# Performance work log

Measured on AMD Instinct MI355X. Metric: run time of the kernel, lower is better.

## Reference

```python
import jax, jax.numpy as jnp
import numpy as np

B, T, H, E = 256, 256, 512, 96  # batch, enc seq len, hidden/enc dim, charset size


def setup_inputs() -> dict:
    key = jax.random.key(0)
    ks = jax.random.split(key, 9)
    s = 0.05  # param scale
    return {
        "prev_h": jax.random.normal(ks[0], (B, H), jnp.float32),
        "prev_c": jax.random.normal(ks[1], (B, H), jnp.float32),
        "batch_H": jax.random.normal(ks[2], (B, T, H), jnp.float32),
        "char_onehots": jax.nn.one_hot(jax.random.randint(ks[3], (B,), 0, E), E, dtype=jnp.float32),
        "W_i2h": jax.random.normal(ks[4], (H, H), jnp.float32) * s,
        "W_h2h": jax.random.normal(ks[5], (H, H), jnp.float32) * s,
        "b_h2h": jnp.zeros((H,), jnp.float32),
        "w_score": jax.random.normal(ks[6], (H, 1), jnp.float32) * s,
        "W_lstm": jax.random.normal(ks[7], (H + E, 4 * H), jnp.float32) * s,
        "U_lstm": jax.random.normal(ks[8], (H, 4 * H), jnp.float32) * s,
        "b_lstm": jnp.zeros((4 * H,), jnp.float32),
    }


def reference(prev_h, prev_c, batch_H, char_onehots,
              W_i2h, W_h2h, b_h2h, w_score, W_lstm, U_lstm, b_lstm):
    # Additive (Bahdanau) attention
    proj = jnp.einsum('btd,dh->bth', batch_H, W_i2h)          # [B,T,H]
    hp = prev_h @ W_h2h + b_h2h                               # [B,H]
    e = jnp.tanh(proj + hp[:, None, :]) @ w_score             # [B,T,1]
    alpha = jax.nn.softmax(e, axis=1)                         # [B,T,1]
    context = jnp.einsum('bt,btd->bd', alpha[..., 0], batch_H)  # [B,D]
    x = jnp.concatenate([context, char_onehots], axis=1)      # [B,D+E]
    # Keras LSTMCell: gate order i, f, c(g), o
    z = x @ W_lstm + prev_h @ U_lstm + b_lstm                 # [B,4H]
    i, f, g, o = jnp.split(z, 4, axis=1)
    c_new = jax.nn.sigmoid(f) * prev_c + jax.nn.sigmoid(i) * jnp.tanh(g)
    h_new = jax.nn.sigmoid(o) * jnp.tanh(c_new)
    return h_new, c_new, alpha
```

## Files before the change

kernel.cpp:

```cpp
#include <hip/hip_runtime.h>
#include <hip/hip_bf16.h>
#include <math.h>

#define Bq 256
#define Tq 256
#define Hq 512
#define Eq 96

typedef __attribute__((ext_vector_type(8))) short short8;
typedef __attribute__((ext_vector_type(4))) float f32x4;

static __device__ __forceinline__ unsigned short f2bf(float f) {
  union { float f; unsigned u; } v; v.f = f;
  unsigned r = v.u + 0x7FFF + ((v.u >> 16) & 1);
  return (unsigned short)(r >> 16);
}

static __device__ __forceinline__ ushort4 pack4(float4 v) {
  ushort4 p;
  p.x = f2bf(v.x); p.y = f2bf(v.y); p.z = f2bf(v.z); p.w = f2bf(v.w);
  return p;
}

static __device__ __forceinline__ short8 pack8(float4 a, float4 b) {
  union { short8 s; ushort4 u[2]; } r;
  r.u[0] = pack4(a); r.u[1] = pack4(b);
  return r.s;
}

static __device__ __forceinline__ float sat_tanh(float x) {
  float ax = fminf(fabsf(x), 15.0f);
  float e = __builtin_exp2f(ax * 2.885390082f);
  float t = 1.0f - 2.0f / (e + 1.0f);
  return copysignf(t, x);
}

static __device__ __forceinline__ float sat_sig(float x) {
  float cx = fmaxf(fminf(x, 30.0f), -30.0f);
  return 1.0f / (1.0f + __builtin_exp2f(-cx * 1.442695041f));
}

__global__ __launch_bounds__(256) void convW_k(const float* __restrict__ W,
                                               unsigned short* __restrict__ Wt) {
  __shared__ float tile[32][33];
  int bx = blockIdx.x & 15, by = blockIdx.x >> 4;
  int tx = threadIdx.x & 31, ty = threadIdx.x >> 5;
  #pragma unroll
  for (int i = 0; i < 32; i += 8)
    tile[ty + i][tx] = W[(size_t)(by * 32 + ty + i) * Hq + bx * 32 + tx];
  __syncthreads();
  #pragma unroll
  for (int i = 0; i < 32; i += 8)
    Wt[(size_t)(bx * 32 + ty + i) * Hq + by * 32 + tx] = f2bf(tile[tx][ty + i]);
}

__global__ __launch_bounds__(256) void hsplit_k(const float* __restrict__ ph,
                                                const float* __restrict__ Whh,
                                                float* __restrict__ hp) {
  __shared__ __align__(16) float xs[8][128];
  const int ks = blockIdx.x & 3;
  const int nc = (blockIdx.x >> 2) & 3;
  const int bg = blockIdx.x >> 4;
  const int tid = threadIdx.x;
  const int row0 = bg * 8;
  const int d0 = ks * 128;
  for (int i = tid; i < 8 * 32; i += 256) {
    int r = i >> 5, dd = (i & 31) * 4;
    *(float4*)&xs[r][dd] = *(const float4*)&ph[(size_t)(row0 + r) * Hq + d0 + dd];
  }
  __syncthreads();
  const int rt = tid >> 6;
  const int ct = tid & 63;
  const int n = nc * 128 + ct * 2;
  float a00 = 0, a01 = 0, a10 = 0, a11 = 0;
  for (int dd = 0; dd < 128; dd += 4) {
    float4 x0 = *(const float4*)&xs[rt * 2][dd];
    float4 x1 = *(const float4*)&xs[rt * 2 + 1][dd];
    #pragma unroll
    for (int j = 0; j < 4; j++) {
      float2 w = *(const float2*)&Whh[(size_t)(d0 + dd + j) * Hq + n];
      float xj0 = ((const float*)&x0)[j];
      float xj1 = ((const float*)&x1)[j];
      a00 += xj0 * w.x; a01 += xj0 * w.y;
      a10 += xj1 * w.x; a11 += xj1 * w.y;
    }
  }
  int row = row0 + rt * 2;
  atomicAdd(&hp[(size_t)row * Hq + n], a00);
  atomicAdd(&hp[(size_t)row * Hq + n + 1], a01);
  atomicAdd(&hp[(size_t)(row + 1) * Hq + n], a10);
  atomicAdd(&hp[(size_t)(row + 1) * Hq + n + 1], a11);
}

#define LDKA 72

__global__ __launch_bounds__(512) void fused_score5_k(
    const float* __restrict__ A,
    const unsigned short* __restrict__ Wt,
    const float* __restrict__ hp,
    const float* __restrict__ bh,
    const float* __restrict__ wsc,
    float* __restrict__ e) {
  __shared__ unsigned short As[2][128 * LDKA];
  __shared__ unsigned short Bs[2][128 * LDKA];
  __shared__ float red[8][64];

  const int tid = threadIdx.x;
  const int n0 = blockIdx.x * 128;
  const int m0 = blockIdx.y * 128;
  const int b = m0 >> 8;
  const int wave = tid >> 6;
  const int lane = tid & 63;
  const int quad = lane >> 4;
  const int l16 = lane & 15;
  const int wm = wave >> 2;
  const int wn4 = wave & 3;

  const int arow = tid >> 2, aq = tid & 3;
  const float* Agp = A + (size_t)(m0 + arow) * Hq + aq * 16;
  const unsigned short* Bgp = Wt + (size_t)(n0 + arow) * Hq + aq * 16;

  f32x4 acc[4][2] = {};

  {
    float4 a0[4]; uint4 b0[2];
    #pragma unroll
    for (int q = 0; q < 4; q++) a0[q] = *(const float4*)(Agp + q * 4);
    b0[0] = *(const uint4*)(Bgp);
    b0[1] = *(const uint4*)(Bgp + 8);
    *(short8*)&As[0][arow * LDKA + aq * 16] = pack8(a0[0], a0[1]);
    *(short8*)&As[0][arow * LDKA + aq * 16 + 8] = pack8(a0[2], a0[3]);
    *(uint4*)&Bs[0][arow * LDKA + aq * 16] = b0[0];
    *(uint4*)&Bs[0][arow * LDKA + aq * 16 + 8] = b0[1];
  }
  __syncthreads();

  int cur = 0;
  for (int ks = 0; ks < 8; ks++) {
    float4 aN[4]; uint4 bN[2];
    if (ks < 7) {
      const int k1 = (ks + 1) * 64;
      #pragma unroll
      for (int q = 0; q < 4; q++) aN[q] = *(const float4*)(Agp + k1 + q * 4);
      bN[0] = *(const uint4*)(Bgp + k1);
      bN[1] = *(const uint4*)(Bgp + k1 + 8);
    }

    short8 af[4][2], bf[2][2];
    #pragma unroll
    for (int mi = 0; mi < 4; mi++)
      #pragma unroll
      for (int k2 = 0; k2 < 2; k2++)
        af[mi][k2] = *(const short8*)&As[cur][(wm * 64 + mi * 16 + l16) * LDKA + k2 * 32 + quad * 8];
    #pragma unroll
    for (int ni = 0; ni < 2; ni++)
      #pragma unroll
      for (int k2 = 0; k2 < 2; k2++)
        bf[ni][k2] = *(const short8*)&Bs[cur][(wn4 * 32 + ni * 16 + l16) * LDKA + k2 * 32 + quad * 8];

    #pragma unroll
    for (int k2 = 0; k2 < 2; k2++)
      #pragma unroll
      for (int mi = 0; mi < 4; mi++)
        #pragma unroll
        for (int ni = 0; ni < 2; ni++)
          acc[mi][ni] = __builtin_amdgcn_mfma_f32_16x16x32_bf16(
              af[mi][k2], bf[ni][k2], acc[mi][ni], 0, 0, 0);

    if (ks < 7) {
      *(short8*)&As[cur ^ 1][arow * LDKA + aq * 16] = pack8(aN[0], aN[1]);
      *(short8*)&As[cur ^ 1][arow * LDKA + aq * 16 + 8] = pack8(aN[2], aN[3]);
      *(uint4*)&Bs[cur ^ 1][arow * LDKA + aq * 16] = bN[0];
      *(uint4*)&Bs[cur ^ 1][arow * LDKA + aq * 16 + 8] = bN[1];
    }
    __syncthreads();
    cur ^= 1;
  }

  float hv[2], wv[2];
  #pragma unroll
  for (int ni = 0; ni < 2; ni++) {
    int c = n0 + wn4 * 32 + ni * 16 + l16;
    hv[ni] = hp[(size_t)b * Hq + c] + bh[c];
    wv[ni] = wsc[c];
  }
  #pragma unroll
  for (int mi = 0; mi < 4; mi++) {
    float s[4] = {0, 0, 0, 0};
    #pragma unroll
    for (int ni = 0; ni < 2; ni++)
      #pragma unroll
      for (int r = 0; r < 4; r++)
        s[r] += sat_tanh(acc[mi][ni][r] + hv[ni]) * wv[ni];
    #pragma unroll
    for (int r = 0; r < 4; r++) {
      s[r] += __shfl_xor(s[r], 8, 64);
      s[r] += __shfl_xor(s[r], 4, 64);
      s[r] += __shfl_xor(s[r], 2, 64);
      s[r] += __shfl_xor(s[r], 1, 64);
    }
    if (l16 == 0) {
      #pragma unroll
      for (int r = 0; r < 4; r++) red[wave][mi * 16 + quad * 4 + r] = s[r];
    }
  }
  __syncthreads();
  if (tid < 128) {
    const int half = tid >> 6, ri = tid & 63;
    float t = red[half * 4 + 0][ri] + red[half * 4 + 1][ri] +
              red[half * 4 + 2][ri] + red[half * 4 + 3][ri];
    atomicAdd(&e[m0 + tid], t);
  }
}

__global__ __launch_bounds__(256) void softmax_k(float* __restrict__ ea) {
  __shared__ float red[8];
  int b = blockIdx.x, t = threadIdx.x;
  int wave = t >> 6, lane = t & 63;
  float x = ea[b * Tq + t];
  float m = x;
  #pragma unroll
  for (int off = 32; off >= 1; off >>= 1) m = fmaxf(m, __shfl_xor(m, off, 64));
  if (lane == 0) red[wave] = m;
  __syncthreads();
  m = fmaxf(fmaxf(red[0], red[1]), fmaxf(red[2], red[3]));
  float ex = __builtin_exp2f((x - m) * 1.442695041f);
  float s = ex;
  #pragma unroll
  for (int off = 32; off >= 1; off >>= 1) s += __shfl_xor(s, off, 64);
  if (lane == 0) red[4 + wave] = s;
  __syncthreads();
  s = red[4] + red[5] + red[6] + red[7];
  ea[b * Tq + t] = ex / s;
}

__global__ __launch_bounds__(256) void ctxsplit_k(const float* __restrict__ alpha,
                                                  const float* __restrict__ bH,
                                                  float* __restrict__ ctx) {
  __shared__ float al[64];
  const int b = blockIdx.x >> 2;
  const int tc = blockIdx.x & 3;
  const int tid = threadIdx.x;
  if (tid < 64) al[tid] = alpha[b * Tq + tc * 64 + tid];
  __syncthreads();
  const float2* Hp = (const float2*)(bH + (size_t)b * Tq * Hq + (size_t)tc * 64 * Hq);
  float ax = 0.f, ay = 0.f;
  #pragma unroll 8
  for (int t = 0; t < 64; t++) {
    float a = al[t];
    float2 v = Hp[t * (Hq / 2) + tid];
    ax += a * v.x;
    ay += a * v.y;
  }
  atomicAdd(&ctx[(size_t)b * Hq + 2 * tid], ax);
  atomicAdd(&ctx[(size_t)b * Hq + 2 * tid + 1], ay);
}

__global__ __launch_bounds__(256) void zsplit_k(
    const float* __restrict__ ctx, const float* __restrict__ oneh,
    const float* __restrict__ ph, const float* __restrict__ Wl,
    const float* __restrict__ Ul, float* __restrict__ z) {
  __shared__ __align__(16) float xs[32 * 280];
  const int ks = blockIdx.x & 3;
  const int hc = (blockIdx.x >> 2) & 7;
  const int bg = blockIdx.x >> 5;
  const int tid = threadIdx.x;
  const int row0 = bg * 32;
  const int dbase = ks * 280;

  for (int i = tid; i < 32 * 280; i += 256) {
    int r = i / 280, dd = i % 280;
    int g = dbase + dd;
    float v;
    if (g < 512) v = ctx[(size_t)(row0 + r) * Hq + g];
    else if (g < 608) v = oneh[(row0 + r) * Eq + (g - 512)];
    else v = ph[(size_t)(row0 + r) * Hq + (g - 608)];
    xs[r * 280 + dd] = v;
  }
  __syncthreads();

  const int rt = tid >> 6;
  const int ct = tid & 63;
  const int c0 = ct * 4;
  const int gate = c0 >> 6;
  const int ho = c0 & 63;
  const int n = gate * 512 + hc * 64 + ho;

  float acc[8][4] = {};
  for (int dd = 0; dd < 280; dd += 4) {
    float4 xr[8];
    #pragma unroll
    for (int r = 0; r < 8; r++)
      xr[r] = *(const float4*)&xs[(rt * 8 + r) * 280 + dd];
    #pragma unroll
    for (int j = 0; j < 4; j++) {
      int g = dbase + dd + j;
      const float* wp = (g < 608) ? &Wl[(size_t)g * 2048 + n]
                                  : &Ul[(size_t)(g - 608) * 2048 + n];
      float4 w = *(const float4*)wp;
      #pragma unroll
      for (int r = 0; r < 8; r++) {
        float x = ((const float*)&xr[r])[j];
        acc[r][0] += x * w.x; acc[r][1] += x * w.y;
        acc[r][2] += x * w.z; acc[r][3] += x * w.w;
      }
    }
  }
  #pragma unroll
  for (int r = 0; r < 8; r++) {
    float* zp = &z[(size_t)(row0 + rt * 8 + r) * 2048 + n];
    #pragma unroll
    for (int j = 0; j < 4; j++) atomicAdd(zp + j, acc[r][j]);
  }
}

__global__ __launch_bounds__(256) void gatesz_k(const float* __restrict__ z,
                                                const float* __restrict__ bl,
                                                const float* __restrict__ pc,
                                                float* __restrict__ outh,
                                                float* __restrict__ outc) {
  int p = blockIdx.x * 256 + threadIdx.x;
  #pragma unroll
  for (int q = 0; q < 2; q++, p += 65536) {
    int r = p >> 9, h = p & 511;
    const float* zb = z + (size_t)r * 2048;
    float gi = zb[h] + bl[h];
    float gf = zb[512 + h] + bl[512 + h];
    float gg = zb[1024 + h] + bl[1024 + h];
    float go = zb[1536 + h] + bl[1536 + h];
    float cn = sat_sig(gf) * pc[p] + sat_sig(gi) * sat_tanh(gg);
    float hn = sat_sig(go) * sat_tanh(cn);
    outh[p] = hn;
    outc[p] = cn;
  }
}

#define KXc 1120
__global__ __launch_bounds__(256) void zgates2_k(
    const float* __restrict__ ctx, const float* __restrict__ oneh,
    const float* __restrict__ ph, const float* __restrict__ pc,
    const float* __restrict__ Wl, const float* __restrict__ Ul,
    const float* __restrict__ bl,
    float* __restrict__ outh, float* __restrict__ outc) {
  __shared__ __align__(16) float xs[8 * KXc];
  const int bg = blockIdx.x >> 3;
  const int hc = blockIdx.x & 7;
  const int tid = threadIdx.x;
  const int row0 = bg * 8;

  for (int i = tid; i < 8 * 128; i += 256) {
    int r = i >> 7, dd = (i & 127) * 4;
    *(float4*)&xs[r * KXc + dd] = *(const float4*)&ctx[(size_t)(row0 + r) * Hq + dd];
  }
  for (int i = tid; i < 8 * 128; i += 256) {
    int r = i >> 7, dd = (i & 127) * 4;
    *(float4*)&xs[r * KXc + 608 + dd] = *(const float4*)&ph[(size_t)(row0 + r) * Hq + dd];
  }
  if (tid < 8 * 24) {
    int r = tid / 24, dd = (tid % 24) * 4;
    *(float4*)&xs[r * KXc + 512 + dd] = *(const float4*)&oneh[(row0 + r) * Eq + dd];
  }
  __syncthreads();

  const int rt = tid >> 6;
  const int ct = tid & 63;
  const int c0 = ct * 4;
  const int gate = c0 >> 6;
  const int ho = c0 & 63;
  const int n = gate * 512 + hc * 64 + ho;

  float acc0[4] = {0, 0, 0, 0};
  float acc1[4] = {0, 0, 0, 0};
  const float* xr0 = &xs[(rt * 2) * KXc];
  const float* xr1 = &xs[(rt * 2 + 1) * KXc];

  for (int d = 0; d < 608; d += 4) {
    float4 x0 = *(const float4*)&xr0[d];
    float4 x1 = *(const float4*)&xr1[d];
    #pragma unroll
    for (int j = 0; j < 4; j++) {
      float4 w = *(const float4*)&Wl[(size_t)(d + j) * 2048 + n];
      float a = ((const float*)&x0)[j], b = ((const float*)&x1)[j];
      acc0[0] += a * w.x; acc0[1] += a * w.y; acc0[2] += a * w.z; acc0[3] += a * w.w;
      acc1[0] += b * w.x; acc1[1] += b * w.y; acc1[2] += b * w.z; acc1[3] += b * w.w;
    }
  }
  for (int d = 0; d < 512; d += 4) {
    float4 x0 = *(const float4*)&xr0[608 + d];
    float4 x1 = *(const float4*)&xr1[608 + d];
    #pragma unroll
    for (int j = 0; j < 4; j++) {
      float4 w = *(const float4*)&Ul[(size_t)(d + j) * 2048 + n];
      float a = ((const float*)&x0)[j], b = ((const float*)&x1)[j];
      acc0[0] += a * w.x; acc0[1] += a * w.y; acc0[2] += a * w.z; acc0[3] += a * w.w;
      acc1[0] += b * w.x; acc1[1] += b * w.y; acc1[2] += b * w.z; acc1[3] += b * w.w;
    }
  }

  __syncthreads();
  float* zs = xs;
  #pragma unroll
  for (int j = 0; j < 4; j++) {
    zs[(rt * 2) * 256 + c0 + j] = acc0[j];
    zs[(rt * 2 + 1) * 256 + c0 + j] = acc1[j];
  }
  __syncthreads();

  #pragma unroll
  for (int p = tid; p < 512; p += 256) {
    int r = p >> 6, o = p & 63;
    int h = hc * 64 + o;
    int grow = row0 + r;
    float gi = zs[r * 256 + o]       + bl[h];
    float gf = zs[r * 256 + 64 + o]  + bl[512 + h];
    float gg = zs[r * 256 + 128 + o] + bl[1024 + h];
    float go = zs[r * 256 + 192 + o] + bl[1536 + h];
    float cn = sat_sig(gf) * pc[(size_t)grow * Hq + h] + sat_sig(gi) * sat_tanh(gg);
    float hn = sat_sig(go) * sat_tanh(cn);
    outh[(size_t)grow * Hq + h] = hn;
    outc[(size_t)grow * Hq + h] = cn;
  }
}

extern "C" void kernel_launch(void* const* d_in, const int* in_sizes, int n_in,
                              void* d_out, int out_size, void* d_ws, size_t ws_size,
                              hipStream_t stream) {
  const float* prev_h = (const float*)d_in[0];
  const float* prev_c = (const float*)d_in[1];
  const float* batch_H = (const float*)d_in[2];
  const float* oneh = (const float*)d_in[3];
  const float* W_i2h = (const float*)d_in[4];
  const float* W_h2h = (const float*)d_in[5];
  const float* b_h2h = (const float*)d_in[6];
  const float* w_score = (const float*)d_in[7];
  const float* W_lstm = (const float*)d_in[8];
  const float* U_lstm = (const float*)d_in[9];
  const float* b_lstm = (const float*)d_in[10];

  float* out = (float*)d_out;
  float* outh = out;
  float* outc = out + Bq * Hq;
  float* alpha = out + 2 * Bq * Hq;

  float* ws = (float*)d_ws;
  float* hp = ws;
  float* ctx = ws;
  unsigned short* Wt = (unsigned short*)(ws + 131072);
  float* z = ws + 131072;

  const bool bigws = ws_size >= 2621440;

  hipMemsetAsync(alpha, 0, Bq * Tq * sizeof(float), stream);
  hipMemsetAsync(hp, 0, Bq * Hq * sizeof(float), stream);
  convW_k<<<256, 256, 0, stream>>>(W_i2h, Wt);
  hsplit_k<<<512, 256, 0, stream>>>(prev_h, W_h2h, hp);
  dim3 g5(4, 512);
  fused_score5_k<<<g5, 512, 0, stream>>>(batch_H, Wt, hp, b_h2h, w_score, alpha);
  softmax_k<<<256, 256, 0, stream>>>(alpha);
  if (bigws) {
    hipMemsetAsync(ws, 0, 2621440, stream);
    ctxsplit_k<<<1024, 256, 0, stream>>>(alpha, batch_H, ctx);
    zsplit_k<<<256, 256, 0, stream>>>(ctx, oneh, prev_h, W_lstm, U_lstm, z);
    gatesz_k<<<256, 256, 0, stream>>>(z, b_lstm, prev_c, outh, outc);
  } else {
    hipMemsetAsync(ctx, 0, Bq * Hq * sizeof(float), stream);
    ctxsplit_k<<<1024, 256, 0, stream>>>(alpha, batch_H, ctx);
    zgates2_k<<<256, 256, 0, stream>>>(ctx, oneh, prev_h, prev_c,
                                       W_lstm, U_lstm, b_lstm, outh, outc);
  }
}
```

Measured before the change: 407.4 us.

## Drop atomics in hp GEMM and score partials; remap blocks per XCD

The hidden projection kernel now covers the full K range in each block and writes its results directly, so the memset and float atomics are gone. With a large workspace, the score kernel writes per-N-chunk partial scores to a 4x buffer that a new softmax kernel sums, removing the alpha memset and the atomics there too. Score blocks are remapped on a 1D grid so that consecutive M-tiles, and the four N-chunks sharing each A tile, land on the same XCD for L2 reuse. The trade-offs are fewer, longer hp blocks (128 blocks covering full K) and extra workspace traffic for the partial scores.

```diff
diff --git a/kernel.cpp b/kernel.cpp
--- a/kernel.cpp
+++ b/kernel.cpp
@@ -54,31 +54,29 @@
     Wt[(size_t)(bx * 32 + ty + i) * Hq + by * 32 + tx] = f2bf(tile[tx][ty + i]);
 }
 
-__global__ __launch_bounds__(256) void hsplit_k(const float* __restrict__ ph,
-                                                const float* __restrict__ Whh,
-                                                float* __restrict__ hp) {
-  __shared__ __align__(16) float xs[8][128];
-  const int ks = blockIdx.x & 3;
-  const int nc = (blockIdx.x >> 2) & 3;
-  const int bg = blockIdx.x >> 4;
+__global__ __launch_bounds__(256) void hsplitF_k(const float* __restrict__ ph,
+                                                 const float* __restrict__ Whh,
+                                                 float* __restrict__ hp) {
+  __shared__ __align__(16) float xs[8][512];
+  const int nc = blockIdx.x & 3;
+  const int bg = blockIdx.x >> 2;
   const int tid = threadIdx.x;
   const int row0 = bg * 8;
-  const int d0 = ks * 128;
-  for (int i = tid; i < 8 * 32; i += 256) {
-    int r = i >> 5, dd = (i & 31) * 4;
-    *(float4*)&xs[r][dd] = *(const float4*)&ph[(size_t)(row0 + r) * Hq + d0 + dd];
+  for (int i = tid; i < 8 * 128; i += 256) {
+    int r = i >> 7, dd = (i & 127) * 4;
+    *(float4*)&xs[r][dd] = *(const float4*)&ph[(size_t)(row0 + r) * Hq + dd];
   }
   __syncthreads();
   const int rt = tid >> 6;
   const int ct = tid & 63;
   const int n = nc * 128 + ct * 2;
   float a00 = 0, a01 = 0, a10 = 0, a11 = 0;
-  for (int dd = 0; dd < 128; dd += 4) {
+  for (int dd = 0; dd < 512; dd += 4) {
     float4 x0 = *(const float4*)&xs[rt * 2][dd];
     float4 x1 = *(const float4*)&xs[rt * 2 + 1][dd];
     #pragma unroll
     for (int j = 0; j < 4; j++) {
-      float2 w = *(const float2*)&Whh[(size_t)(d0 + dd + j) * Hq + n];
+      float2 w = *(const float2*)&Whh[(size_t)(dd + j) * Hq + n];
       float xj0 = ((const float*)&x0)[j];
       float xj1 = ((const float*)&x1)[j];
       a00 += xj0 * w.x; a01 += xj0 * w.y;
@@ -86,28 +84,33 @@
     }
   }
   int row = row0 + rt * 2;
-  atomicAdd(&hp[(size_t)row * Hq + n], a00);
-  atomicAdd(&hp[(size_t)row * Hq + n + 1], a01);
-  atomicAdd(&hp[(size_t)(row + 1) * Hq + n], a10);
-  atomicAdd(&hp[(size_t)(row + 1) * Hq + n + 1], a11);
+  hp[(size_t)row * Hq + n] = a00;
+  hp[(size_t)row * Hq + n + 1] = a01;
+  hp[(size_t)(row + 1) * Hq + n] = a10;
+  hp[(size_t)(row + 1) * Hq + n + 1] = a11;
 }
 
 #define LDKA 72
 
-__global__ __launch_bounds__(512) void fused_score5_k(
+template <int EMODE>
+__global__ __launch_bounds__(512) void fused_score6_k(
     const float* __restrict__ A,
     const unsigned short* __restrict__ Wt,
     const float* __restrict__ hp,
     const float* __restrict__ bh,
     const float* __restrict__ wsc,
-    float* __restrict__ e) {
+    float* __restrict__ eout) {
   __shared__ unsigned short As[2][128 * LDKA];
   __shared__ unsigned short Bs[2][128 * LDKA];
   __shared__ float red[8][64];
 
   const int tid = threadIdx.x;
-  const int n0 = blockIdx.x * 128;
-  const int m0 = blockIdx.y * 128;
+  const int wg = blockIdx.x;
+  const int xcd = wg & 7;
+  const int local = wg >> 3;
+  const int nch = local & 3;
+  const int m0 = (xcd * 64 + (local >> 2)) * 128;
+  const int n0 = nch * 128;
   const int b = m0 >> 8;
   const int wave = tid >> 6;
   const int lane = tid & 63;
@@ -209,8 +212,34 @@
     const int half = tid >> 6, ri = tid & 63;
     float t = red[half * 4 + 0][ri] + red[half * 4 + 1][ri] +
               red[half * 4 + 2][ri] + red[half * 4 + 3][ri];
-    atomicAdd(&e[m0 + tid], t);
-  }
+    if (EMODE == 0)
+      eout[(size_t)nch * (Bq * Tq) + m0 + tid] = t;
+    else
+      atomicAdd(&eout[m0 + tid], t);
+  }
+}
+
+__global__ __launch_bounds__(256) void softmax4_k(const float* __restrict__ e4,
+                                                  float* __restrict__ alpha) {
+  __shared__ float red[8];
+  int b = blockIdx.x, t = threadIdx.x;
+  int wave = t >> 6, lane = t & 63;
+  int idx = b * Tq + t;
+  float x = e4[idx] + e4[Bq * Tq + idx] + e4[2 * Bq * Tq + idx] + e4[3 * Bq * Tq + idx];
+  float m = x;
+  #pragma unroll
+  for (int off = 32; off >= 1; off >>= 1) m = fmaxf(m, __shfl_xor(m, off, 64));
+  if (lane == 0) red[wave] = m;
+  __syncthreads();
+  m = fmaxf(fmaxf(red[0], red[1]), fmaxf(red[2], red[3]));
+  float ex = __builtin_exp2f((x - m) * 1.442695041f);
+  float s = ex;
+  #pragma unroll
+  for (int off = 32; off >= 1; off >>= 1) s += __shfl_xor(s, off, 64);
+  if (lane == 0) red[4 + wave] = s;
+  __syncthreads();
+  s = red[4] + red[5] + red[6] + red[7];
+  alpha[idx] = ex / s;
 }
 
 __global__ __launch_bounds__(256) void softmax_k(float* __restrict__ ea) {
@@ -443,26 +472,35 @@
   float* alpha = out + 2 * Bq * Hq;
 
   float* ws = (float*)d_ws;
-  float* hp = ws;
-  float* ctx = ws;
-  unsigned short* Wt = (unsigned short*)(ws + 131072);
-  float* z = ws + 131072;
-
   const bool bigws = ws_size >= 2621440;
 
-  hipMemsetAsync(alpha, 0, Bq * Tq * sizeof(float), stream);
-  hipMemsetAsync(hp, 0, Bq * Hq * sizeof(float), stream);
-  convW_k<<<256, 256, 0, stream>>>(W_i2h, Wt);
-  hsplit_k<<<512, 256, 0, stream>>>(prev_h, W_h2h, hp);
-  dim3 g5(4, 512);
-  fused_score5_k<<<g5, 512, 0, stream>>>(batch_H, Wt, hp, b_h2h, w_score, alpha);
-  softmax_k<<<256, 256, 0, stream>>>(alpha);
   if (bigws) {
+    float* hp = ws;
+    float* e4 = ws + 131072;
+    unsigned short* Wt = (unsigned short*)(ws + 393216);
+    float* ctx = ws;
+    float* z = ws + 131072;
+
+    hsplitF_k<<<128, 256, 0, stream>>>(prev_h, W_h2h, hp);
+    convW_k<<<256, 256, 0, stream>>>(W_i2h, Wt);
+    fused_score6_k<0><<<2048, 512, 0, stream>>>(batch_H, Wt, hp, b_h2h,
+                                                w_score, e4);
+    softmax4_k<<<256, 256, 0, stream>>>(e4, alpha);
     hipMemsetAsync(ws, 0, 2621440, stream);
     ctxsplit_k<<<1024, 256, 0, stream>>>(alpha, batch_H, ctx);
     zsplit_k<<<256, 256, 0, stream>>>(ctx, oneh, prev_h, W_lstm, U_lstm, z);
     gatesz_k<<<256, 256, 0, stream>>>(z, b_lstm, prev_c, outh, outc);
   } else {
+    float* hp = ws;
+    unsigned short* Wt = (unsigned short*)(ws + 131072);
+    float* ctx = ws;
+
+    hipMemsetAsync(alpha, 0, Bq * Tq * sizeof(float), stream);
+    hsplitF_k<<<128, 256, 0, stream>>>(prev_h, W_h2h, hp);
+    convW_k<<<256, 256, 0, stream>>>(W_i2h, Wt);
+    fused_score6_k<1><<<2048, 512, 0, stream>>>(batch_H, Wt, hp, b_h2h,
+                                                w_score, alpha);
+    softmax_k<<<256, 256, 0, stream>>>(alpha);
     hipMemsetAsync(ctx, 0, Bq * Hq * sizeof(float), stream);
     ctxsplit_k<<<1024, 256, 0, stream>>>(alpha, batch_H, ctx);
     zgates2_k<<<256, 256, 0, stream>>>(ctx, oneh, prev_h, prev_c,
```

New measurement: 423.0 us. 3.8% more time.
